# Optimization experiments

Measured on AMD Instinct MI355X. Metric: run time of the kernel, lower is better.

## Reference

```python
import jax, jax.numpy as jnp
import numpy as np

OBS_DIM = 256
HIDDEN = 512

def setup_inputs() -> dict:
    key = jax.random.key(0)
    ks = jax.random.split(key, 7)
    s_x = 1.0 / np.sqrt(OBS_DIM)
    s_h = 1.0 / np.sqrt(HIDDEN)
    return {
        "x": jax.random.normal(ks[0], (32, 2048, OBS_DIM), dtype=jnp.float32),
        "Whx_w": jax.random.uniform(ks[1], (HIDDEN, OBS_DIM), jnp.float32, -s_x, s_x),
        "Whx_b": jax.random.uniform(ks[2], (HIDDEN,), jnp.float32, -s_x, s_x),
        "Whh_w": jax.random.uniform(ks[3], (HIDDEN, HIDDEN), jnp.float32, -s_h, s_h),
        "Whh_b": jax.random.uniform(ks[4], (HIDDEN,), jnp.float32, -s_h, s_h),
        "Woh_w": jax.random.uniform(ks[5], (HIDDEN, HIDDEN), jnp.float32, -s_h, s_h),
        "Woh_b": jax.random.uniform(ks[6], (HIDDEN,), jnp.float32, -s_h, s_h),
    }

def reference(x, Whx_w, Whx_b, Whh_w, Whh_b, Woh_w, Woh_b):
    # x: (B, L, D). Precompute input projection for all timesteps (one big GEMM).
    B, L, D = x.shape
    xp = jnp.einsum("bld,hd->blh", x, Whx_w) + Whx_b  # (B, L, H)

    def step(h_prev, xp_t):
        h_t = jax.nn.relu(xp_t + h_prev @ Whh_w.T + Whh_b)
        y_t = jax.nn.softmax(h_t @ Woh_w.T + Woh_b, axis=1)
        return h_t, (y_t, h_t)

    h0 = jnp.zeros((B, HIDDEN), dtype=x.dtype)
    _, (ys, hs) = jax.lax.scan(step, h0, jnp.swapaxes(xp, 0, 1))  # scan over L
    output_arr = jnp.swapaxes(ys, 0, 1)  # (B, L, H)
    hidden_arr = jnp.swapaxes(hs, 0, 1)  # (B, L, H)
    return output_arr, hidden_arr
```

## Files before the change

### kernel.cpp

```cpp
#include <hip/hip_runtime.h>

#define H    512
#define DOBS 256
#define BATCH 32
#define SEQ  2048
#define NSLICE 8
#define NS 64

typedef float f8 __attribute__((ext_vector_type(8)));

__global__ __launch_bounds__(256) void transpose_k(const float* __restrict__ W,
                                                   float* __restrict__ Wt) {
  __shared__ float tile[32][33];
  int tx  = threadIdx.x & 31;
  int ty4 = (threadIdx.x >> 5) * 4;
  int bx = blockIdx.x * 32;
  int by = blockIdx.y * 32;
#pragma unroll
  for (int i = 0; i < 4; ++i)
    tile[ty4 + i][tx] = W[(by + ty4 + i) * H + bx + tx];
  __syncthreads();
#pragma unroll
  for (int i = 0; i < 4; ++i)
    Wt[(bx + ty4 + i) * H + by + tx] = tile[tx][ty4 + i];
}

__global__ __launch_bounds__(256) void gemm_bias_k(const float* __restrict__ A,
                                                   const float* __restrict__ B,
                                                   const float* __restrict__ bias,
                                                   float* __restrict__ C,
                                                   int M, int N, int K) {
  __shared__ float As[32][68];
  __shared__ float Bs[32][68];
  const int m0 = blockIdx.x * 64;
  const int n0 = blockIdx.y * 64;
  const int t  = threadIdx.x;
  const int tm = (t >> 4) * 4;
  const int tn = (t & 15) * 4;
  const int lrow = t >> 3;
  const int lcol = (t & 7) * 4;

  float acc[4][4] = {};

  for (int k0 = 0; k0 < K; k0 += 32) {
    float4 a0 = *(const float4*)&A[(size_t)(m0 + lrow)      * K + k0 + lcol];
    float4 a1 = *(const float4*)&A[(size_t)(m0 + lrow + 32) * K + k0 + lcol];
    float4 b0 = *(const float4*)&B[(size_t)(n0 + lrow)      * K + k0 + lcol];
    float4 b1 = *(const float4*)&B[(size_t)(n0 + lrow + 32) * K + k0 + lcol];
    __syncthreads();
    As[lcol + 0][lrow] = a0.x; As[lcol + 1][lrow] = a0.y;
    As[lcol + 2][lrow] = a0.z; As[lcol + 3][lrow] = a0.w;
    As[lcol + 0][lrow + 32] = a1.x; As[lcol + 1][lrow + 32] = a1.y;
    As[lcol + 2][lrow + 32] = a1.z; As[lcol + 3][lrow + 32] = a1.w;
    Bs[lcol + 0][lrow] = b0.x; Bs[lcol + 1][lrow] = b0.y;
    Bs[lcol + 2][lrow] = b0.z; Bs[lcol + 3][lrow] = b0.w;
    Bs[lcol + 0][lrow + 32] = b1.x; Bs[lcol + 1][lrow + 32] = b1.y;
    Bs[lcol + 2][lrow + 32] = b1.z; Bs[lcol + 3][lrow + 32] = b1.w;
    __syncthreads();
#pragma unroll
    for (int k = 0; k < 32; ++k) {
      float4 a = *(const float4*)&As[k][tm];
      float4 b = *(const float4*)&Bs[k][tn];
      acc[0][0] = fmaf(a.x, b.x, acc[0][0]);
      acc[0][1] = fmaf(a.x, b.y, acc[0][1]);
      acc[0][2] = fmaf(a.x, b.z, acc[0][2]);
      acc[0][3] = fmaf(a.x, b.w, acc[0][3]);
      acc[1][0] = fmaf(a.y, b.x, acc[1][0]);
      acc[1][1] = fmaf(a.y, b.y, acc[1][1]);
      acc[1][2] = fmaf(a.y, b.z, acc[1][2]);
      acc[1][3] = fmaf(a.y, b.w, acc[1][3]);
      acc[2][0] = fmaf(a.z, b.x, acc[2][0]);
      acc[2][1] = fmaf(a.z, b.y, acc[2][1]);
      acc[2][2] = fmaf(a.z, b.z, acc[2][2]);
      acc[2][3] = fmaf(a.z, b.w, acc[2][3]);
      acc[3][0] = fmaf(a.w, b.x, acc[3][0]);
      acc[3][1] = fmaf(a.w, b.y, acc[3][1]);
      acc[3][2] = fmaf(a.w, b.z, acc[3][2]);
      acc[3][3] = fmaf(a.w, b.w, acc[3][3]);
    }
  }

  float4 b4 = *(const float4*)&bias[n0 + tn];
#pragma unroll
  for (int i = 0; i < 4; ++i) {
    float4 c;
    c.x = acc[i][0] + b4.x;
    c.y = acc[i][1] + b4.y;
    c.z = acc[i][2] + b4.z;
    c.w = acc[i][3] + b4.w;
    *(float4*)&C[(size_t)(m0 + tm + i) * N + n0 + tn] = c;
  }
}

__global__ __launch_bounds__(256, 1) void rnn_rec_k(float* __restrict__ hid,
                                                    float* __restrict__ exch,
                                                    const float* __restrict__ Wt,
                                                    const float* __restrict__ bias) {
  const int b     = blockIdx.x & (BATCH - 1);
  const int slice = blockIdx.x >> 5;
  const int n0    = slice * NS;
  const int tid   = threadIdx.x;
  const int w     = tid >> 6;
  const int l     = tid & 63;

  __shared__ __align__(16) float shh[H];
  __shared__ float sh_part[2][4][NS];

  float* hb = hid  + (size_t)b * SEQ * H;
  float* eb = exch + (size_t)b * SEQ * H;

  f8 Wv[16];
  {
    const float* wp = Wt + (size_t)(w * 128) * H + n0 + l;
#pragma unroll
    for (int i = 0; i < 16; ++i) {
#pragma unroll
      for (int j = 0; j < 8; ++j)
        Wv[i][j] = wp[(size_t)(i * 8 + j) * H];
    }
  }
  const float bn = bias[n0 + l];

  const float4* sh4 = (const float4*)&shh[w * 128];

  for (int t = 0; t < SEQ; ++t) {
    float xp = 0.f;
    if (w == 0) xp = hb[(size_t)t * H + n0 + l];

    float partial = 0.f;
    if (t > 0) {
      const float* ep = eb + (size_t)(t - 1) * H + w * 128;
      float v0, v1;
      for (;;) {
        v0 = __hip_atomic_load(ep + l,      __ATOMIC_RELAXED, __HIP_MEMORY_SCOPE_AGENT);
        v1 = __hip_atomic_load(ep + 64 + l, __ATOMIC_RELAXED, __HIP_MEMORY_SCOPE_AGENT);
        if (!__any(!(v0 >= 1.0f && v1 >= 1.0f))) break;
      }
      shh[w * 128 + l]      = v0 - 1.0f;
      shh[w * 128 + 64 + l] = v1 - 1.0f;
      asm volatile("s_waitcnt lgkmcnt(0)" ::: "memory");

      float a0 = 0.f, a1 = 0.f, a2 = 0.f, a3 = 0.f;
#pragma unroll
      for (int i = 0; i < 16; ++i) {
        float4 hA = sh4[2 * i];
        float4 hB = sh4[2 * i + 1];
        a0 = fmaf(Wv[i][0], hA.x, a0);
        a1 = fmaf(Wv[i][1], hA.y, a1);
        a2 = fmaf(Wv[i][2], hA.z, a2);
        a3 = fmaf(Wv[i][3], hA.w, a3);
        a0 = fmaf(Wv[i][4], hB.x, a0);
        a1 = fmaf(Wv[i][5], hB.y, a1);
        a2 = fmaf(Wv[i][6], hB.z, a2);
        a3 = fmaf(Wv[i][7], hB.w, a3);
      }
      partial = (a0 + a1) + (a2 + a3);
    }

    sh_part[t & 1][w][l] = partial;
    __syncthreads();

    if (w == 0) {
      float v = sh_part[t & 1][0][l] + sh_part[t & 1][1][l]
              + sh_part[t & 1][2][l] + sh_part[t & 1][3][l] + xp + bn;
      float hv = fmaxf(v, 0.f);
      __hip_atomic_store(&eb[(size_t)t * H + n0 + l], hv + 1.0f,
                         __ATOMIC_RELAXED, __HIP_MEMORY_SCOPE_AGENT);
      hb[(size_t)t * H + n0 + l] = hv;
    }
  }
}

__global__ __launch_bounds__(256) void softmax_k(float* __restrict__ Z) {
  __shared__ float smax[4];
  __shared__ float ssum[4];
  float* row = Z + (size_t)blockIdx.x * H;
  const int t = threadIdx.x;
  float2 v = *(float2*)&row[2 * t];
  float m = fmaxf(v.x, v.y);
#pragma unroll
  for (int o = 32; o > 0; o >>= 1) m = fmaxf(m, __shfl_xor(m, o, 64));
  const int wave = t >> 6, lane = t & 63;
  if (lane == 0) smax[wave] = m;
  __syncthreads();
  m = fmaxf(fmaxf(smax[0], smax[1]), fmaxf(smax[2], smax[3]));
  const float LOG2E = 1.44269504088896f;
  float ex = exp2f((v.x - m) * LOG2E);
  float ey = exp2f((v.y - m) * LOG2E);
  float s = ex + ey;
#pragma unroll
  for (int o = 32; o > 0; o >>= 1) s += __shfl_xor(s, o, 64);
  if (lane == 0) ssum[wave] = s;
  __syncthreads();
  float inv = 1.0f / (ssum[0] + ssum[1] + ssum[2] + ssum[3]);
  float2 r;
  r.x = ex * inv;
  r.y = ey * inv;
  *(float2*)&row[2 * t] = r;
}

extern "C" void kernel_launch(void* const* d_in, const int* in_sizes, int n_in,
                              void* d_out, int out_size, void* d_ws, size_t ws_size,
                              hipStream_t stream) {
  const float* x     = (const float*)d_in[0];
  const float* Whx_w = (const float*)d_in[1];
  const float* Whx_b = (const float*)d_in[2];
  const float* Whh_w = (const float*)d_in[3];
  const float* Whh_b = (const float*)d_in[4];
  const float* Woh_w = (const float*)d_in[5];
  const float* Woh_b = (const float*)d_in[6];

  float* y   = (float*)d_out;
  float* hid = (float*)d_out + (size_t)BATCH * SEQ * H;
  float* Wt  = (float*)d_ws;

  const int M = BATCH * SEQ;

  transpose_k<<<dim3(16, 16), 256, 0, stream>>>(Whh_w, Wt);
  gemm_bias_k<<<dim3(M / 64, H / 64), 256, 0, stream>>>(x, Whx_w, Whx_b, hid, M, H, DOBS);
  rnn_rec_k<<<BATCH * NSLICE, 256, 0, stream>>>(hid, y, Wt, Whh_b);
  gemm_bias_k<<<dim3(M / 64, H / 64), 256, 0, stream>>>(hid, Woh_w, Woh_b, y, M, H, H);
  softmax_k<<<M, 256, 0, stream>>>(y);
}
```

Before: 4.362 ms.

## Remove block barrier from recurrence via per-wave full-h copy and shuffle reduction

Each wave now owns 16 output neurons, and each group of 4 lanes splits the 512-long dot product, reducing with shuffles instead of combining partials through shared memory and a __syncthreads. Every wave polls and loads the whole previous hidden vector itself, and the next step's input projection is prefetched a step ahead. A prefetch load of the exchange row for the current step is also issued early. Weights are read row-wise straight from Whh, so the transpose kernel is dropped. This removes the per-step block barrier from the serial chain, at the cost of each wave polling 512 values, four times as much redundant global traffic per step.

```diff
diff --git a/kernel.cpp b/kernel.cpp
--- a/kernel.cpp
+++ b/kernel.cpp
@@ -4,26 +4,8 @@
 #define DOBS 256
 #define BATCH 32
 #define SEQ  2048
-#define NSLICE 8
-#define NS 64
 
 typedef float f8 __attribute__((ext_vector_type(8)));
-
-__global__ __launch_bounds__(256) void transpose_k(const float* __restrict__ W,
-                                                   float* __restrict__ Wt) {
-  __shared__ float tile[32][33];
-  int tx  = threadIdx.x & 31;
-  int ty4 = (threadIdx.x >> 5) * 4;
-  int bx = blockIdx.x * 32;
-  int by = blockIdx.y * 32;
-#pragma unroll
-  for (int i = 0; i < 4; ++i)
-    tile[ty4 + i][tx] = W[(by + ty4 + i) * H + bx + tx];
-  __syncthreads();
-#pragma unroll
-  for (int i = 0; i < 4; ++i)
-    Wt[(bx + ty4 + i) * H + by + tx] = tile[tx][ty4 + i];
-}
 
 __global__ __launch_bounds__(256) void gemm_bias_k(const float* __restrict__ A,
                                                    const float* __restrict__ B,
@@ -94,80 +76,95 @@
 
 __global__ __launch_bounds__(256, 1) void rnn_rec_k(float* __restrict__ hid,
                                                     float* __restrict__ exch,
-                                                    const float* __restrict__ Wt,
+                                                    const float* __restrict__ W,
                                                     const float* __restrict__ bias) {
-  const int b     = blockIdx.x & (BATCH - 1);
-  const int slice = blockIdx.x >> 5;
-  const int n0    = slice * NS;
-  const int tid   = threadIdx.x;
-  const int w     = tid >> 6;
-  const int l     = tid & 63;
-
-  __shared__ __align__(16) float shh[H];
-  __shared__ float sh_part[2][4][NS];
+  const int b    = blockIdx.x & (BATCH - 1);
+  const int sgrp = blockIdx.x >> 5;
+  const int tid  = threadIdx.x;
+  const int w    = tid >> 6;
+  const int l    = tid & 63;
+  const int c    = l & 3;
+  const int oo   = l >> 2;
+  const int nout = sgrp * 64 + w * 16 + oo;
+  const bool lead = (c == 0);
+
+  __shared__ __align__(16) float shh[4][4 * 132];
 
   float* hb = hid  + (size_t)b * SEQ * H;
   float* eb = exch + (size_t)b * SEQ * H;
 
   f8 Wv[16];
   {
-    const float* wp = Wt + (size_t)(w * 128) * H + n0 + l;
-#pragma unroll
-    for (int i = 0; i < 16; ++i) {
-#pragma unroll
-      for (int j = 0; j < 8; ++j)
-        Wv[i][j] = wp[(size_t)(i * 8 + j) * H];
-    }
-  }
-  const float bn = bias[n0 + l];
-
-  const float4* sh4 = (const float4*)&shh[w * 128];
+    const float* wp = W + (size_t)nout * H + c * 128;
+#pragma unroll
+    for (int i = 0; i < 16; ++i) Wv[i] = *(const f8*)(wp + 8 * i);
+  }
+  const float bn = bias[nout];
+
+  float* shw = shh[w];
+  float* swr = shw + 8 * l + ((l >> 4) << 2);
+  const float* srd = shw + c * 132;
+
+  float xp_next = lead ? hb[nout] : 0.f;
 
   for (int t = 0; t < SEQ; ++t) {
-    float xp = 0.f;
-    if (w == 0) xp = hb[(size_t)t * H + n0 + l];
-
-    float partial = 0.f;
+    const float xp = xp_next;
+    {
+      const int tn = (t + 1 < SEQ) ? t + 1 : t;
+      if (lead) xp_next = hb[(size_t)tn * H + nout];
+    }
+    float pfv = __hip_atomic_load(eb + (size_t)t * H + 8 * l,
+                                  __ATOMIC_RELAXED, __HIP_MEMORY_SCOPE_AGENT);
+
+    float r = 0.f;
     if (t > 0) {
-      const float* ep = eb + (size_t)(t - 1) * H + w * 128;
-      float v0, v1;
+      float* ep = eb + (size_t)(t - 1) * H + 8 * l;
+      float v0, v1, v2, v3, v4, v5, v6, v7;
       for (;;) {
-        v0 = __hip_atomic_load(ep + l,      __ATOMIC_RELAXED, __HIP_MEMORY_SCOPE_AGENT);
-        v1 = __hip_atomic_load(ep + 64 + l, __ATOMIC_RELAXED, __HIP_MEMORY_SCOPE_AGENT);
-        if (!__any(!(v0 >= 1.0f && v1 >= 1.0f))) break;
+        v0 = __hip_atomic_load(ep + 0, __ATOMIC_RELAXED, __HIP_MEMORY_SCOPE_AGENT);
+        v1 = __hip_atomic_load(ep + 1, __ATOMIC_RELAXED, __HIP_MEMORY_SCOPE_AGENT);
+        v2 = __hip_atomic_load(ep + 2, __ATOMIC_RELAXED, __HIP_MEMORY_SCOPE_AGENT);
+        v3 = __hip_atomic_load(ep + 3, __ATOMIC_RELAXED, __HIP_MEMORY_SCOPE_AGENT);
+        v4 = __hip_atomic_load(ep + 4, __ATOMIC_RELAXED, __HIP_MEMORY_SCOPE_AGENT);
+        v5 = __hip_atomic_load(ep + 5, __ATOMIC_RELAXED, __HIP_MEMORY_SCOPE_AGENT);
+        v6 = __hip_atomic_load(ep + 6, __ATOMIC_RELAXED, __HIP_MEMORY_SCOPE_AGENT);
+        v7 = __hip_atomic_load(ep + 7, __ATOMIC_RELAXED, __HIP_MEMORY_SCOPE_AGENT);
+        bool ok = (v0 >= 1.f) & (v1 >= 1.f) & (v2 >= 1.f) & (v3 >= 1.f) &
+                  (v4 >= 1.f) & (v5 >= 1.f) & (v6 >= 1.f) & (v7 >= 1.f);
+        if (!__any(!ok)) break;
       }
-      shh[w * 128 + l]      = v0 - 1.0f;
-      shh[w * 128 + 64 + l] = v1 - 1.0f;
+      float4 hA = {v0 - 1.f, v1 - 1.f, v2 - 1.f, v3 - 1.f};
+      float4 hB = {v4 - 1.f, v5 - 1.f, v6 - 1.f, v7 - 1.f};
+      *(float4*)swr = hA;
+      *(float4*)(swr + 4) = hB;
       asm volatile("s_waitcnt lgkmcnt(0)" ::: "memory");
 
       float a0 = 0.f, a1 = 0.f, a2 = 0.f, a3 = 0.f;
 #pragma unroll
       for (int i = 0; i < 16; ++i) {
-        float4 hA = sh4[2 * i];
-        float4 hB = sh4[2 * i + 1];
-        a0 = fmaf(Wv[i][0], hA.x, a0);
-        a1 = fmaf(Wv[i][1], hA.y, a1);
-        a2 = fmaf(Wv[i][2], hA.z, a2);
-        a3 = fmaf(Wv[i][3], hA.w, a3);
-        a0 = fmaf(Wv[i][4], hB.x, a0);
-        a1 = fmaf(Wv[i][5], hB.y, a1);
-        a2 = fmaf(Wv[i][6], hB.z, a2);
-        a3 = fmaf(Wv[i][7], hB.w, a3);
+        float4 x0 = *(const float4*)(srd + 8 * i);
+        float4 x1 = *(const float4*)(srd + 8 * i + 4);
+        a0 = fmaf(Wv[i][0], x0.x, a0);
+        a1 = fmaf(Wv[i][1], x0.y, a1);
+        a2 = fmaf(Wv[i][2], x0.z, a2);
+        a3 = fmaf(Wv[i][3], x0.w, a3);
+        a0 = fmaf(Wv[i][4], x1.x, a0);
+        a1 = fmaf(Wv[i][5], x1.y, a1);
+        a2 = fmaf(Wv[i][6], x1.z, a2);
+        a3 = fmaf(Wv[i][7], x1.w, a3);
       }
-      partial = (a0 + a1) + (a2 + a3);
-    }
-
-    sh_part[t & 1][w][l] = partial;
-    __syncthreads();
-
-    if (w == 0) {
-      float v = sh_part[t & 1][0][l] + sh_part[t & 1][1][l]
-              + sh_part[t & 1][2][l] + sh_part[t & 1][3][l] + xp + bn;
-      float hv = fmaxf(v, 0.f);
-      __hip_atomic_store(&eb[(size_t)t * H + n0 + l], hv + 1.0f,
+      r = (a0 + a1) + (a2 + a3);
+      r += __shfl_xor(r, 1, 64);
+      r += __shfl_xor(r, 2, 64);
+    }
+
+    if (lead) {
+      float hv = fmaxf(r + xp + bn, 0.f);
+      __hip_atomic_store(&eb[(size_t)t * H + nout], hv + 1.0f,
                          __ATOMIC_RELAXED, __HIP_MEMORY_SCOPE_AGENT);
-      hb[(size_t)t * H + n0 + l] = hv;
-    }
+      hb[(size_t)t * H + nout] = hv;
+    }
+    asm volatile("" :: "v"(pfv));
   }
 }
 
@@ -212,13 +209,11 @@
 
   float* y   = (float*)d_out;
   float* hid = (float*)d_out + (size_t)BATCH * SEQ * H;
-  float* Wt  = (float*)d_ws;
 
   const int M = BATCH * SEQ;
 
-  transpose_k<<<dim3(16, 16), 256, 0, stream>>>(Whh_w, Wt);
   gemm_bias_k<<<dim3(M / 64, H / 64), 256, 0, stream>>>(x, Whx_w, Whx_b, hid, M, H, DOBS);
-  rnn_rec_k<<<BATCH * NSLICE, 256, 0, stream>>>(hid, y, Wt, Whh_b);
+  rnn_rec_k<<<BATCH * 8, 256, 0, stream>>>(hid, y, Whh_w, Whh_b);
   gemm_bias_k<<<dim3(M / 64, H / 64), 256, 0, stream>>>(hid, Woh_w, Woh_b, y, M, H, H);
   softmax_k<<<M, 256, 0, stream>>>(y);
 }
```

New measurement: 8.997 ms. 106% more time.

## Enlarge GEMM tiles to 128x128 and prefetch next-step data in RNN recurrence

Applied to the files above, without the earlier changes.

The GEMM kernel moves from 64x64 tiles with 4x4 per-thread outputs to 128x128 tiles with 8x8 per-thread outputs. This raises arithmetic intensity per shared-memory load at the cost of more registers. The recurrent kernel now issues a plain load of the next step's exchange line (to warm the cache) and the next step's input projection before the matvec, so their latency overlaps compute. The __syncthreads is replaced by an explicit lgkmcnt wait plus s_barrier. Most of the time is in the sequential recurrence, so its per-step latency decides the outcome.

```diff
diff --git a/kernel.cpp b/kernel.cpp
--- a/kernel.cpp
+++ b/kernel.cpp
@@ -30,65 +30,61 @@
                                                    const float* __restrict__ bias,
                                                    float* __restrict__ C,
                                                    int M, int N, int K) {
-  __shared__ float As[32][68];
-  __shared__ float Bs[32][68];
-  const int m0 = blockIdx.x * 64;
-  const int n0 = blockIdx.y * 64;
+  __shared__ float As[16][132];
+  __shared__ float Bs[16][132];
+  const int m0 = blockIdx.x * 128;
+  const int n0 = blockIdx.y * 128;
   const int t  = threadIdx.x;
   const int tm = (t >> 4) * 4;
   const int tn = (t & 15) * 4;
-  const int lrow = t >> 3;
-  const int lcol = (t & 7) * 4;
-
-  float acc[4][4] = {};
-
-  for (int k0 = 0; k0 < K; k0 += 32) {
+  const int lrow = t >> 2;
+  const int lcol = (t & 3) * 4;
+
+  float acc[8][8] = {};
+
+  for (int k0 = 0; k0 < K; k0 += 16) {
     float4 a0 = *(const float4*)&A[(size_t)(m0 + lrow)      * K + k0 + lcol];
-    float4 a1 = *(const float4*)&A[(size_t)(m0 + lrow + 32) * K + k0 + lcol];
+    float4 a1 = *(const float4*)&A[(size_t)(m0 + lrow + 64) * K + k0 + lcol];
     float4 b0 = *(const float4*)&B[(size_t)(n0 + lrow)      * K + k0 + lcol];
-    float4 b1 = *(const float4*)&B[(size_t)(n0 + lrow + 32) * K + k0 + lcol];
+    float4 b1 = *(const float4*)&B[(size_t)(n0 + lrow + 64) * K + k0 + lcol];
     __syncthreads();
     As[lcol + 0][lrow] = a0.x; As[lcol + 1][lrow] = a0.y;
     As[lcol + 2][lrow] = a0.z; As[lcol + 3][lrow] = a0.w;
-    As[lcol + 0][lrow + 32] = a1.x; As[lcol + 1][lrow + 32] = a1.y;
-    As[lcol + 2][lrow + 32] = a1.z; As[lcol + 3][lrow + 32] = a1.w;
+    As[lcol + 0][lrow + 64] = a1.x; As[lcol + 1][lrow + 64] = a1.y;
+    As[lcol + 2][lrow + 64] = a1.z; As[lcol + 3][lrow + 64] = a1.w;
     Bs[lcol + 0][lrow] = b0.x; Bs[lcol + 1][lrow] = b0.y;
     Bs[lcol + 2][lrow] = b0.z; Bs[lcol + 3][lrow] = b0.w;
-    Bs[lcol + 0][lrow + 32] = b1.x; Bs[lcol + 1][lrow + 32] = b1.y;
-    Bs[lcol + 2][lrow + 32] = b1.z; Bs[lcol + 3][lrow + 32] = b1.w;
+    Bs[lcol + 0][lrow + 64] = b1.x; Bs[lcol + 1][lrow + 64] = b1.y;
+    Bs[lcol + 2][lrow + 64] = b1.z; Bs[lcol + 3][lrow + 64] = b1.w;
     __syncthreads();
 #pragma unroll
-    for (int k = 0; k < 32; ++k) {
-      float4 a = *(const float4*)&As[k][tm];
-      float4 b = *(const float4*)&Bs[k][tn];
-      acc[0][0] = fmaf(a.x, b.x, acc[0][0]);
-      acc[0][1] = fmaf(a.x, b.y, acc[0][1]);
-      acc[0][2] = fmaf(a.x, b.z, acc[0][2]);
-      acc[0][3] = fmaf(a.x, b.w, acc[0][3]);
-      acc[1][0] = fmaf(a.y, b.x, acc[1][0]);
-      acc[1][1] = fmaf(a.y, b.y, acc[1][1]);
-      acc[1][2] = fmaf(a.y, b.z, acc[1][2]);
-      acc[1][3] = fmaf(a.y, b.w, acc[1][3]);
-      acc[2][0] = fmaf(a.z, b.x, acc[2][0]);
-      acc[2][1] = fmaf(a.z, b.y, acc[2][1]);
-      acc[2][2] = fmaf(a.z, b.z, acc[2][2]);
-      acc[2][3] = fmaf(a.z, b.w, acc[2][3]);
-      acc[3][0] = fmaf(a.w, b.x, acc[3][0]);
-      acc[3][1] = fmaf(a.w, b.y, acc[3][1]);
-      acc[3][2] = fmaf(a.w, b.z, acc[3][2]);
-      acc[3][3] = fmaf(a.w, b.w, acc[3][3]);
-    }
-  }
-
-  float4 b4 = *(const float4*)&bias[n0 + tn];
-#pragma unroll
-  for (int i = 0; i < 4; ++i) {
-    float4 c;
-    c.x = acc[i][0] + b4.x;
-    c.y = acc[i][1] + b4.y;
-    c.z = acc[i][2] + b4.z;
-    c.w = acc[i][3] + b4.w;
-    *(float4*)&C[(size_t)(m0 + tm + i) * N + n0 + tn] = c;
+    for (int k = 0; k < 16; ++k) {
+      float4 aA = *(const float4*)&As[k][tm];
+      float4 aB = *(const float4*)&As[k][tm + 64];
+      float4 bA = *(const float4*)&Bs[k][tn];
+      float4 bB = *(const float4*)&Bs[k][tn + 64];
+      float av[8] = {aA.x, aA.y, aA.z, aA.w, aB.x, aB.y, aB.z, aB.w};
+      float bv[8] = {bA.x, bA.y, bA.z, bA.w, bB.x, bB.y, bB.z, bB.w};
+#pragma unroll
+      for (int i = 0; i < 8; ++i)
+#pragma unroll
+        for (int j = 0; j < 8; ++j)
+          acc[i][j] = fmaf(av[i], bv[j], acc[i][j]);
+    }
+  }
+
+  float4 bbA = *(const float4*)&bias[n0 + tn];
+  float4 bbB = *(const float4*)&bias[n0 + tn + 64];
+#pragma unroll
+  for (int i = 0; i < 8; ++i) {
+    int row = m0 + ((i < 4) ? (tm + i) : (64 + tm + i - 4));
+    float4 c0, c1;
+    c0.x = acc[i][0] + bbA.x; c0.y = acc[i][1] + bbA.y;
+    c0.z = acc[i][2] + bbA.z; c0.w = acc[i][3] + bbA.w;
+    c1.x = acc[i][4] + bbB.x; c1.y = acc[i][5] + bbB.y;
+    c1.z = acc[i][6] + bbB.z; c1.w = acc[i][7] + bbB.w;
+    *(float4*)&C[(size_t)row * N + n0 + tn]      = c0;
+    *(float4*)&C[(size_t)row * N + n0 + tn + 64] = c1;
   }
 }
 
@@ -123,23 +119,36 @@
 
   const float4* sh4 = (const float4*)&shh[w * 128];
 
+  float xp_cur = 0.f, xp_nxt = 0.f;
+  if (w == 0) xp_cur = hb[n0 + l];
+  float kp0 = 0.f, kp1 = 0.f;
+
   for (int t = 0; t < SEQ; ++t) {
-    float xp = 0.f;
-    if (w == 0) xp = hb[(size_t)t * H + n0 + l];
-
-    float partial = 0.f;
+    float v0 = 0.f, v1 = 0.f;
     if (t > 0) {
       const float* ep = eb + (size_t)(t - 1) * H + w * 128;
-      float v0, v1;
       for (;;) {
         v0 = __hip_atomic_load(ep + l,      __ATOMIC_RELAXED, __HIP_MEMORY_SCOPE_AGENT);
         v1 = __hip_atomic_load(ep + 64 + l, __ATOMIC_RELAXED, __HIP_MEMORY_SCOPE_AGENT);
         if (!__any(!(v0 >= 1.0f && v1 >= 1.0f))) break;
       }
+      asm volatile("" :: "v"(kp0), "v"(kp1) : "memory");
       shh[w * 128 + l]      = v0 - 1.0f;
       shh[w * 128 + 64 + l] = v1 - 1.0f;
       asm volatile("s_waitcnt lgkmcnt(0)" ::: "memory");
-
+    } else {
+      asm volatile("" ::: "memory");
+    }
+
+    if (t + 1 < SEQ) {
+      const float* pf = eb + (size_t)t * H + w * 128;
+      kp0 = pf[l];
+      kp1 = pf[64 + l];
+      if (w == 0) xp_nxt = hb[(size_t)(t + 1) * H + n0 + l];
+    }
+
+    float partial = 0.f;
+    if (t > 0) {
       float a0 = 0.f, a1 = 0.f, a2 = 0.f, a3 = 0.f;
 #pragma unroll
       for (int i = 0; i < 16; ++i) {
@@ -158,16 +167,19 @@
     }
 
     sh_part[t & 1][w][l] = partial;
-    __syncthreads();
+    asm volatile("s_waitcnt lgkmcnt(0)" ::: "memory");
+    __builtin_amdgcn_s_barrier();
+    asm volatile("" ::: "memory");
 
     if (w == 0) {
       float v = sh_part[t & 1][0][l] + sh_part[t & 1][1][l]
-              + sh_part[t & 1][2][l] + sh_part[t & 1][3][l] + xp + bn;
+              + sh_part[t & 1][2][l] + sh_part[t & 1][3][l] + xp_cur + bn;
       float hv = fmaxf(v, 0.f);
       __hip_atomic_store(&eb[(size_t)t * H + n0 + l], hv + 1.0f,
                          __ATOMIC_RELAXED, __HIP_MEMORY_SCOPE_AGENT);
       hb[(size_t)t * H + n0 + l] = hv;
     }
+    xp_cur = xp_nxt;
   }
 }
 
@@ -217,8 +229,8 @@
   const int M = BATCH * SEQ;
 
   transpose_k<<<dim3(16, 16), 256, 0, stream>>>(Whh_w, Wt);
-  gemm_bias_k<<<dim3(M / 64, H / 64), 256, 0, stream>>>(x, Whx_w, Whx_b, hid, M, H, DOBS);
+  gemm_bias_k<<<dim3(M / 128, H / 128), 256, 0, stream>>>(x, Whx_w, Whx_b, hid, M, H, DOBS);
   rnn_rec_k<<<BATCH * NSLICE, 256, 0, stream>>>(hid, y, Wt, Whh_b);
-  gemm_bias_k<<<dim3(M / 64, H / 64), 256, 0, stream>>>(hid, Woh_w, Woh_b, y, M, H, H);
+  gemm_bias_k<<<dim3(M / 128, H / 128), 256, 0, stream>>>(hid, Woh_w, Woh_b, y, M, H, H);
   softmax_k<<<M, 256, 0, stream>>>(y);
 }
```

New measurement: 3.577 ms. 1.22x faster.
